# Optimization experiments

Measured on AMD Instinct MI355X. Metric: run time of the kernel, lower is better.

## Reference

```python
import jax, jax.numpy as jnp
import numpy as np

N = 500000       # total nodes
D = 256          # input_dim
H = 128          # hidden_dim
G = 4096         # number of graphs (batch.max()+1)


def setup_inputs() -> dict:
    key = jax.random.key(0)
    k_x, k_b, k_w1, k_b1, k_w2, k_b2 = jax.random.split(key, 6)
    x = jax.random.normal(k_x, (N, D), dtype=jnp.float32)
    batch = jnp.sort(jax.random.randint(k_b, (N,), 0, G)).astype(jnp.int64)
    batch = batch.at[-1].set(G - 1)  # ensure batch.max()+1 == G
    s1 = 1.0 / np.sqrt(D)
    s2 = 1.0 / np.sqrt(H)
    W1 = jax.random.uniform(k_w1, (D, H), jnp.float32, -s1, s1)
    b1 = jax.random.uniform(k_b1, (H,), jnp.float32, -s1, s1)
    W2 = jax.random.uniform(k_w2, (H, 1), jnp.float32, -s2, s2)
    b2 = jax.random.uniform(k_b2, (1,), jnp.float32, -s2, s2)
    return {"x": x, "batch": batch, "W1": W1, "b1": b1, "W2": W2, "b2": b2}


def reference(x, batch, W1, b1, W2, b2):
    # attention MLP: Linear -> Tanh -> Linear(->1)
    h = jnp.tanh(x @ W1 + b1)                  # [N, H]
    logits = (h @ W2 + b2)[:, 0]               # [N]
    # per-graph (segment) softmax over nodes
    m = jax.ops.segment_max(logits, batch, num_segments=G)       # [G]
    e = jnp.exp(logits - m[batch])                               # [N]
    denom = jax.ops.segment_sum(e, batch, num_segments=G)        # [G]
    w = e / denom[batch]                                         # [N]
    # weighted sum per graph; empty graphs -> zeros (matches torch branch)
    pooled = jax.ops.segment_sum(x * w[:, None], batch, num_segments=G)  # [G, D]
    return pooled
```

## Files before the change

### kernel.cpp

```cpp
#include <hip/hip_runtime.h>
#include <math.h>

#define D_DIM 256
#define H_DIM 128
#define TILE  32
#define HPAD  264

typedef __attribute__((ext_vector_type(8))) short bf16x8;
typedef __attribute__((ext_vector_type(4))) float f32x4;

__device__ __forceinline__ unsigned short f32_to_bf16(float f) {
  unsigned int u = __float_as_uint(f);
  u += 0x7FFFu + ((u >> 16) & 1u);
  return (unsigned short)(u >> 16);
}

__device__ __forceinline__ unsigned int pack_hi2(float f0, float f1, float& r0, float& r1) {
  unsigned int u0 = __float_as_uint(f0) & 0xFFFF0000u;
  unsigned int u1 = __float_as_uint(f1) & 0xFFFF0000u;
  r0 = f0 - __uint_as_float(u0);
  r1 = f1 - __uint_as_float(u1);
  return (u0 >> 16) | u1;
}
__device__ __forceinline__ unsigned int pack_lo2(float r0, float r1) {
  return (__float_as_uint(r0) >> 16) | (__float_as_uint(r1) & 0xFFFF0000u);
}

__device__ __forceinline__ float tanh_fast(float x) {
  float e = __expf(2.0f * x);
  return 1.0f - 2.0f / (e + 1.0f);
}

__global__ void setup_w1_kernel(const float* __restrict__ W1,
                                unsigned short* __restrict__ wfrag)
{
  const int t = threadIdx.x;
  const int l = t & 63, w = t >> 6;
  const int q = l >> 4, c = l & 15;
#pragma unroll
  for (int kt = 0; kt < 8; ++kt)
#pragma unroll
    for (int nt = 0; nt < 2; ++nt) {
      int f = kt * 2 + nt;
      int col = w * 32 + nt * 16 + c;
#pragma unroll
      for (int j = 0; j < 8; ++j) {
        int k = kt * 32 + q * 8 + j;
        wfrag[((size_t)f * 256 + t) * 8 + j] = f32_to_bf16(W1[k * H_DIM + col]);
      }
    }
}

__global__ void offsets_kernel(const void* __restrict__ batch, int* __restrict__ start,
                               int N, int G)
{
  int g = blockIdx.x * blockDim.x + threadIdx.x;
  if (g > G) return;
  const int* b32 = (const int*)batch;
  bool is64 = (b32[N - 1] != G - 1);
  int lo = 0, hi = N;
  while (lo < hi) {
    int mid = (lo + hi) >> 1;
    long long v = is64 ? ((const long long*)batch)[mid] : (long long)b32[mid];
    if (v < (long long)g) lo = mid + 1; else hi = mid;
  }
  start[g] = lo;
}

__global__ __launch_bounds__(256, 4)
void fused_kernel(const float* __restrict__ x, const unsigned short* __restrict__ wfrag,
                  const float* __restrict__ b1, const float* __restrict__ W2,
                  const int* __restrict__ start, float* __restrict__ out, int N)
{
  __shared__ unsigned short xhi[TILE][HPAD];
  __shared__ unsigned short xlo[TILE][HPAD];
  __shared__ float part[4][TILE];

  const int g = blockIdx.x;
  const int tid = threadIdx.x;
  const int s = start[g], e = start[g + 1];
  if (s >= e) { out[(size_t)g * D_DIM + tid] = 0.0f; return; }
  const int len = e - s;

  const int lane = tid & 63, w = tid >> 6;
  const int q = lane >> 4, c = lane & 15;

  bf16x8 wf[8][2];
#pragma unroll
  for (int kt = 0; kt < 8; ++kt)
#pragma unroll
    for (int nt = 0; nt < 2; ++nt)
      wf[kt][nt] = ((const bf16x8*)wfrag)[(kt * 2 + nt) * 256 + tid];

  float b1c[2], w2c[2];
#pragma unroll
  for (int nt = 0; nt < 2; ++nt) {
    int col = w * 32 + nt * 16 + c;
    b1c[nt] = b1[col];
    w2c[nt] = W2[col];
  }

  float m_run = -INFINITY, Z = 0.0f, accd = 0.0f;

  const int nT = (len + TILE - 1) / TILE;
  for (int ti = 0; ti < nT; ++ti) {
    const int t0 = ti * TILE;
    const int iend = min(TILE, len - t0);

#pragma unroll
    for (int it = 0; it < 4; ++it) {
      int id = tid + 256 * it;
      int row = id >> 5, col8 = (id & 31) * 8;
      int gr = min(s + t0 + row, N - 1);
      const float4* gp = reinterpret_cast<const float4*>(x + (size_t)gr * D_DIM + col8);
      float4 A = gp[0], B = gp[1];
      float r0, r1, r2, r3, r4, r5, r6, r7;
      uint4 H, L;
      H.x = pack_hi2(A.x, A.y, r0, r1);
      H.y = pack_hi2(A.z, A.w, r2, r3);
      H.z = pack_hi2(B.x, B.y, r4, r5);
      H.w = pack_hi2(B.z, B.w, r6, r7);
      L.x = pack_lo2(r0, r1);
      L.y = pack_lo2(r2, r3);
      L.z = pack_lo2(r4, r5);
      L.w = pack_lo2(r6, r7);
      *reinterpret_cast<uint4*>(&xhi[row][col8]) = H;
      *reinterpret_cast<uint4*>(&xlo[row][col8]) = L;
    }
    __syncthreads();

    f32x4 acc[2][2];
#pragma unroll
    for (int m = 0; m < 2; ++m)
#pragma unroll
      for (int nt = 0; nt < 2; ++nt) acc[m][nt] = (f32x4){0.f, 0.f, 0.f, 0.f};

#pragma unroll
    for (int kt = 0; kt < 8; ++kt) {
      const int koff = kt * 32 + q * 8;
      bf16x8 ah0 = *reinterpret_cast<const bf16x8*>(&xhi[c][koff]);
      bf16x8 al0 = *reinterpret_cast<const bf16x8*>(&xlo[c][koff]);
      bf16x8 ah1 = *reinterpret_cast<const bf16x8*>(&xhi[16 + c][koff]);
      bf16x8 al1 = *reinterpret_cast<const bf16x8*>(&xlo[16 + c][koff]);
#pragma unroll
      for (int nt = 0; nt < 2; ++nt) {
        acc[0][nt] = __builtin_amdgcn_mfma_f32_16x16x32_bf16(ah0, wf[kt][nt], acc[0][nt], 0, 0, 0);
        acc[0][nt] = __builtin_amdgcn_mfma_f32_16x16x32_bf16(al0, wf[kt][nt], acc[0][nt], 0, 0, 0);
        acc[1][nt] = __builtin_amdgcn_mfma_f32_16x16x32_bf16(ah1, wf[kt][nt], acc[1][nt], 0, 0, 0);
        acc[1][nt] = __builtin_amdgcn_mfma_f32_16x16x32_bf16(al1, wf[kt][nt], acc[1][nt], 0, 0, 0);
      }
    }

#pragma unroll
    for (int m = 0; m < 2; ++m)
#pragma unroll
      for (int r = 0; r < 4; ++r) {
        float v = tanh_fast(acc[m][0][r] + b1c[0]) * w2c[0]
                + tanh_fast(acc[m][1][r] + b1c[1]) * w2c[1];
#pragma unroll
        for (int o = 1; o < 16; o <<= 1) v += __shfl_xor(v, o, 64);
        if (c == 0) part[w][m * 16 + q * 4 + r] = v;
      }
    __syncthreads();

    {
      int i = lane & 31;
      float li = (i < iend) ? (part[0][i] + part[1][i] + part[2][i] + part[3][i])
                            : -INFINITY;
      float tmax = li;
#pragma unroll
      for (int o = 1; o < 64; o <<= 1) tmax = fmaxf(tmax, __shfl_xor(tmax, o, 64));
      float m_new = fmaxf(m_run, tmax);
      float ei = __expf(li - m_new);
      float esum = ei;
#pragma unroll
      for (int o = 1; o < 32; o <<= 1) esum += __shfl_xor(esum, o, 64);
      float scale = __expf(m_run - m_new);
      Z = Z * scale + esum;
      accd *= scale;
      for (int ii = 0; ii < iend; ++ii) {
        float ev = __shfl(ei, ii, 64);
        float xv = __uint_as_float((unsigned int)xhi[ii][tid] << 16)
                 + __uint_as_float((unsigned int)xlo[ii][tid] << 16);
        accd = fmaf(ev, xv, accd);
      }
      m_run = m_new;
    }
    __syncthreads();
  }

  out[(size_t)g * D_DIM + tid] = accd / Z;
}

extern "C" void kernel_launch(void* const* d_in, const int* in_sizes, int n_in,
                              void* d_out, int out_size, void* d_ws, size_t ws_size,
                              hipStream_t stream)
{
  const float* x     = (const float*)d_in[0];
  const void*  batch = d_in[1];
  const float* W1    = (const float*)d_in[2];
  const float* b1    = (const float*)d_in[3];
  const float* W2    = (const float*)d_in[4];

  const int N = in_sizes[0] / D_DIM;
  const int G = out_size / D_DIM;

  unsigned short* wfrag = (unsigned short*)d_ws;
  int* startA = (int*)((char*)d_ws + 16 * 256 * 8 * sizeof(unsigned short));
  float* out = (float*)d_out;

  setup_w1_kernel<<<1, 256, 0, stream>>>(W1, wfrag);
  offsets_kernel<<<(G + 1 + 255) / 256, 256, 0, stream>>>(batch, startA, N, G);
  fused_kernel<<<G, 256, 0, stream>>>(x, wfrag, b1, W2, startA, out, N);
}
```

Before: 200.6 us.

## Prefetch next node tile into registers while computing current tile

Result: slower. 450.0 us (+124.4%).

```diff
diff --git a/kernel.cpp b/kernel.cpp
--- a/kernel.cpp
+++ b/kernel.cpp
@@ -67,7 +67,7 @@
   start[g] = lo;
 }
 
-__global__ __launch_bounds__(256, 4)
+__global__ __launch_bounds__(256, 3)
 void fused_kernel(const float* __restrict__ x, const unsigned short* __restrict__ wfrag,
                   const float* __restrict__ b1, const float* __restrict__ W2,
                   const int* __restrict__ start, float* __restrict__ out, int N)
@@ -84,6 +84,7 @@
 
   const int lane = tid & 63, w = tid >> 6;
   const int q = lane >> 4, c = lane & 15;
+  const int srow = tid >> 5, scol8 = (tid & 31) * 8;
 
   bf16x8 wf[8][2];
 #pragma unroll
@@ -101,33 +102,42 @@
   }
 
   float m_run = -INFINITY, Z = 0.0f, accd = 0.0f;
-
   const int nT = (len + TILE - 1) / TILE;
+
+#pragma unroll
+  for (int it = 0; it < 4; ++it) {
+    int row = srow + it * 8;
+    int gr = min(s + row, N - 1);
+    const float4* gp = reinterpret_cast<const float4*>(x + (size_t)gr * D_DIM + scol8);
+    float4 A = gp[0], B = gp[1];
+    float r0, r1, r2, r3, r4, r5, r6, r7;
+    uint4 H, L;
+    H.x = pack_hi2(A.x, A.y, r0, r1);  H.y = pack_hi2(A.z, A.w, r2, r3);
+    H.z = pack_hi2(B.x, B.y, r4, r5);  H.w = pack_hi2(B.z, B.w, r6, r7);
+    L.x = pack_lo2(r0, r1);  L.y = pack_lo2(r2, r3);
+    L.z = pack_lo2(r4, r5);  L.w = pack_lo2(r6, r7);
+    *reinterpret_cast<uint4*>(&xhi[row][scol8]) = H;
+    *reinterpret_cast<uint4*>(&xlo[row][scol8]) = L;
+  }
+
   for (int ti = 0; ti < nT; ++ti) {
     const int t0 = ti * TILE;
     const int iend = min(TILE, len - t0);
-
-#pragma unroll
-    for (int it = 0; it < 4; ++it) {
-      int id = tid + 256 * it;
-      int row = id >> 5, col8 = (id & 31) * 8;
-      int gr = min(s + t0 + row, N - 1);
-      const float4* gp = reinterpret_cast<const float4*>(x + (size_t)gr * D_DIM + col8);
-      float4 A = gp[0], B = gp[1];
-      float r0, r1, r2, r3, r4, r5, r6, r7;
-      uint4 H, L;
-      H.x = pack_hi2(A.x, A.y, r0, r1);
-      H.y = pack_hi2(A.z, A.w, r2, r3);
-      H.z = pack_hi2(B.x, B.y, r4, r5);
-      H.w = pack_hi2(B.z, B.w, r6, r7);
-      L.x = pack_lo2(r0, r1);
-      L.y = pack_lo2(r2, r3);
-      L.z = pack_lo2(r4, r5);
-      L.w = pack_lo2(r6, r7);
-      *reinterpret_cast<uint4*>(&xhi[row][col8]) = H;
-      *reinterpret_cast<uint4*>(&xlo[row][col8]) = L;
-    }
+    const bool haveNext = (ti + 1 < nT);
+
     __syncthreads();
+
+    float4 pf[4][2];
+    if (haveNext) {
+#pragma unroll
+      for (int it = 0; it < 4; ++it) {
+        int row = srow + it * 8;
+        int gr = min(s + t0 + TILE + row, N - 1);
+        const float4* gp = reinterpret_cast<const float4*>(x + (size_t)gr * D_DIM + scol8);
+        pf[it][0] = gp[0];
+        pf[it][1] = gp[1];
+      }
+    }
 
     f32x4 acc[2][2];
 #pragma unroll
@@ -164,12 +174,12 @@
     __syncthreads();
 
     {
-      int i = lane & 31;
+      const int i = lane & 31;
       float li = (i < iend) ? (part[0][i] + part[1][i] + part[2][i] + part[3][i])
                             : -INFINITY;
       float tmax = li;
 #pragma unroll
-      for (int o = 1; o < 64; o <<= 1) tmax = fmaxf(tmax, __shfl_xor(tmax, o, 64));
+      for (int o = 1; o < 32; o <<= 1) tmax = fmaxf(tmax, __shfl_xor(tmax, o, 64));
       float m_new = fmaxf(m_run, tmax);
       float ei = __expf(li - m_new);
       float esum = ei;
@@ -177,16 +187,47 @@
       for (int o = 1; o < 32; o <<= 1) esum += __shfl_xor(esum, o, 64);
       float scale = __expf(m_run - m_new);
       Z = Z * scale + esum;
-      accd *= scale;
-      for (int ii = 0; ii < iend; ++ii) {
-        float ev = __shfl(ei, ii, 64);
-        float xv = __uint_as_float((unsigned int)xhi[ii][tid] << 16)
-                 + __uint_as_float((unsigned int)xlo[ii][tid] << 16);
-        accd = fmaf(ev, xv, accd);
-      }
+
+      float ac0 = 0.f, ac1 = 0.f, ac2 = 0.f, ac3 = 0.f;
+#pragma unroll
+      for (int ii = 0; ii < TILE; ii += 4) {
+        float e0 = __shfl(ei, ii + 0, 64);
+        float e1 = __shfl(ei, ii + 1, 64);
+        float e2 = __shfl(ei, ii + 2, 64);
+        float e3 = __shfl(ei, ii + 3, 64);
+        float x0 = __uint_as_float((unsigned int)xhi[ii + 0][tid] << 16)
+                 + __uint_as_float((unsigned int)xlo[ii + 0][tid] << 16);
+        float x1 = __uint_as_float((unsigned int)xhi[ii + 1][tid] << 16)
+                 + __uint_as_float((unsigned int)xlo[ii + 1][tid] << 16);
+        float x2 = __uint_as_float((unsigned int)xhi[ii + 2][tid] << 16)
+                 + __uint_as_float((unsigned int)xlo[ii + 2][tid] << 16);
+        float x3 = __uint_as_float((unsigned int)xhi[ii + 3][tid] << 16)
+                 + __uint_as_float((unsigned int)xlo[ii + 3][tid] << 16);
+        ac0 = fmaf(e0, x0, ac0);
+        ac1 = fmaf(e1, x1, ac1);
+        ac2 = fmaf(e2, x2, ac2);
+        ac3 = fmaf(e3, x3, ac3);
+      }
+      accd = fmaf(accd, scale, (ac0 + ac1) + (ac2 + ac3));
       m_run = m_new;
     }
     __syncthreads();
+
+    if (haveNext) {
+#pragma unroll
+      for (int it = 0; it < 4; ++it) {
+        int row = srow + it * 8;
+        float4 A = pf[it][0], B = pf[it][1];
+        float r0, r1, r2, r3, r4, r5, r6, r7;
+        uint4 H, L;
+        H.x = pack_hi2(A.x, A.y, r0, r1);  H.y = pack_hi2(A.z, A.w, r2, r3);
+        H.z = pack_hi2(B.x, B.y, r4, r5);  H.w = pack_hi2(B.z, B.w, r6, r7);
+        L.x = pack_lo2(r0, r1);  L.y = pack_lo2(r2, r3);
+        L.z = pack_lo2(r4, r5);  L.w = pack_lo2(r6, r7);
+        *reinterpret_cast<uint4*>(&xhi[row][scol8]) = H;
+        *reinterpret_cast<uint4*>(&xlo[row][scol8]) = L;
+      }
+    }
   }
 
   out[(size_t)g * D_DIM + tid] = accd / Z;
```

## Prefetch next x tile into registers, drop bf16 lo split, accumulate in fp32

Applied to the files above, without the earlier changes.

Measured after the change: 226.2 us. 12.8% more time.

```diff
diff --git a/kernel.cpp b/kernel.cpp
--- a/kernel.cpp
+++ b/kernel.cpp
@@ -15,15 +15,10 @@
   return (unsigned short)(u >> 16);
 }
 
-__device__ __forceinline__ unsigned int pack_hi2(float f0, float f1, float& r0, float& r1) {
-  unsigned int u0 = __float_as_uint(f0) & 0xFFFF0000u;
-  unsigned int u1 = __float_as_uint(f1) & 0xFFFF0000u;
-  r0 = f0 - __uint_as_float(u0);
-  r1 = f1 - __uint_as_float(u1);
+__device__ __forceinline__ unsigned int pack2_rn(float f0, float f1) {
+  unsigned int u0 = (__float_as_uint(f0) + 0x8000u) & 0xFFFF0000u;
+  unsigned int u1 = (__float_as_uint(f1) + 0x8000u) & 0xFFFF0000u;
   return (u0 >> 16) | u1;
-}
-__device__ __forceinline__ unsigned int pack_lo2(float r0, float r1) {
-  return (__float_as_uint(r0) >> 16) | (__float_as_uint(r1) & 0xFFFF0000u);
 }
 
 __device__ __forceinline__ float tanh_fast(float x) {
@@ -67,14 +62,14 @@
   start[g] = lo;
 }
 
-__global__ __launch_bounds__(256, 4)
+__global__ __launch_bounds__(256, 3)
 void fused_kernel(const float* __restrict__ x, const unsigned short* __restrict__ wfrag,
                   const float* __restrict__ b1, const float* __restrict__ W2,
                   const int* __restrict__ start, float* __restrict__ out, int N)
 {
   __shared__ unsigned short xhi[TILE][HPAD];
-  __shared__ unsigned short xlo[TILE][HPAD];
-  __shared__ float part[4][TILE];
+  __shared__ float part_t[TILE][4];
+  __shared__ float pacc_lds[8][D_DIM];
 
   const int g = blockIdx.x;
   const int tid = threadIdx.x;
@@ -84,92 +79,93 @@
 
   const int lane = tid & 63, w = tid >> 6;
   const int q = lane >> 4, c = lane & 15;
-
-  bf16x8 wf[8][2];
-#pragma unroll
-  for (int kt = 0; kt < 8; ++kt)
-#pragma unroll
-    for (int nt = 0; nt < 2; ++nt)
-      wf[kt][nt] = ((const bf16x8*)wfrag)[(kt * 2 + nt) * 256 + tid];
-
-  float b1c[2], w2c[2];
-#pragma unroll
-  for (int nt = 0; nt < 2; ++nt) {
-    int col = w * 32 + nt * 16 + c;
-    b1c[nt] = b1[col];
-    w2c[nt] = W2[col];
-  }
-
-  float m_run = -INFINITY, Z = 0.0f, accd = 0.0f;
+  const int srow = tid >> 5;
+  const int scol8 = (tid & 31) * 8;
+
+  const bf16x8* wfv = (const bf16x8*)wfrag;
+
+  float b1c0, b1c1, w2c0, w2c1;
+  {
+    int col0 = w * 32 + c, col1 = w * 32 + 16 + c;
+    b1c0 = b1[col0]; b1c1 = b1[col1];
+    w2c0 = W2[col0]; w2c1 = W2[col1];
+  }
+
+  float m_run = -INFINITY, Z = 0.0f;
+  float pc0 = 0.f, pc1 = 0.f, pc2 = 0.f, pc3 = 0.f,
+        pc4 = 0.f, pc5 = 0.f, pc6 = 0.f, pc7 = 0.f;
+
+  float4 A0, B0, A1, B1, A2, B2, A3, B3;
+  {
+    const float4* p0 = reinterpret_cast<const float4*>(x + (size_t)min(s + srow,      N - 1) * D_DIM + scol8);
+    const float4* p1 = reinterpret_cast<const float4*>(x + (size_t)min(s + srow +  8, N - 1) * D_DIM + scol8);
+    const float4* p2 = reinterpret_cast<const float4*>(x + (size_t)min(s + srow + 16, N - 1) * D_DIM + scol8);
+    const float4* p3 = reinterpret_cast<const float4*>(x + (size_t)min(s + srow + 24, N - 1) * D_DIM + scol8);
+    A0 = p0[0]; B0 = p0[1];
+    A1 = p1[0]; B1 = p1[1];
+    A2 = p2[0]; B2 = p2[1];
+    A3 = p3[0]; B3 = p3[1];
+  }
 
   const int nT = (len + TILE - 1) / TILE;
   for (int ti = 0; ti < nT; ++ti) {
-    const int t0 = ti * TILE;
-    const int iend = min(TILE, len - t0);
-
-#pragma unroll
-    for (int it = 0; it < 4; ++it) {
-      int id = tid + 256 * it;
-      int row = id >> 5, col8 = (id & 31) * 8;
-      int gr = min(s + t0 + row, N - 1);
-      const float4* gp = reinterpret_cast<const float4*>(x + (size_t)gr * D_DIM + col8);
-      float4 A = gp[0], B = gp[1];
-      float r0, r1, r2, r3, r4, r5, r6, r7;
-      uint4 H, L;
-      H.x = pack_hi2(A.x, A.y, r0, r1);
-      H.y = pack_hi2(A.z, A.w, r2, r3);
-      H.z = pack_hi2(B.x, B.y, r4, r5);
-      H.w = pack_hi2(B.z, B.w, r6, r7);
-      L.x = pack_lo2(r0, r1);
-      L.y = pack_lo2(r2, r3);
-      L.z = pack_lo2(r4, r5);
-      L.w = pack_lo2(r6, r7);
-      *reinterpret_cast<uint4*>(&xhi[row][col8]) = H;
-      *reinterpret_cast<uint4*>(&xlo[row][col8]) = L;
+    const int iend = min(TILE, len - ti * TILE);
+
+    {
+      uint4 H;
+      H.x = pack2_rn(A0.x, A0.y); H.y = pack2_rn(A0.z, A0.w);
+      H.z = pack2_rn(B0.x, B0.y); H.w = pack2_rn(B0.z, B0.w);
+      *reinterpret_cast<uint4*>(&xhi[srow][scol8]) = H;
+      H.x = pack2_rn(A1.x, A1.y); H.y = pack2_rn(A1.z, A1.w);
+      H.z = pack2_rn(B1.x, B1.y); H.w = pack2_rn(B1.z, B1.w);
+      *reinterpret_cast<uint4*>(&xhi[srow + 8][scol8]) = H;
+      H.x = pack2_rn(A2.x, A2.y); H.y = pack2_rn(A2.z, A2.w);
+      H.z = pack2_rn(B2.x, B2.y); H.w = pack2_rn(B2.z, B2.w);
+      *reinterpret_cast<uint4*>(&xhi[srow + 16][scol8]) = H;
+      H.x = pack2_rn(A3.x, A3.y); H.y = pack2_rn(A3.z, A3.w);
+      H.z = pack2_rn(B3.x, B3.y); H.w = pack2_rn(B3.z, B3.w);
+      *reinterpret_cast<uint4*>(&xhi[srow + 24][scol8]) = H;
     }
     __syncthreads();
 
-    f32x4 acc[2][2];
-#pragma unroll
-    for (int m = 0; m < 2; ++m)
-#pragma unroll
-      for (int nt = 0; nt < 2; ++nt) acc[m][nt] = (f32x4){0.f, 0.f, 0.f, 0.f};
-
+    f32x4 acc00 = {0.f, 0.f, 0.f, 0.f}, acc01 = {0.f, 0.f, 0.f, 0.f};
+    f32x4 acc10 = {0.f, 0.f, 0.f, 0.f}, acc11 = {0.f, 0.f, 0.f, 0.f};
 #pragma unroll
     for (int kt = 0; kt < 8; ++kt) {
       const int koff = kt * 32 + q * 8;
       bf16x8 ah0 = *reinterpret_cast<const bf16x8*>(&xhi[c][koff]);
-      bf16x8 al0 = *reinterpret_cast<const bf16x8*>(&xlo[c][koff]);
       bf16x8 ah1 = *reinterpret_cast<const bf16x8*>(&xhi[16 + c][koff]);
-      bf16x8 al1 = *reinterpret_cast<const bf16x8*>(&xlo[16 + c][koff]);
-#pragma unroll
-      for (int nt = 0; nt < 2; ++nt) {
-        acc[0][nt] = __builtin_amdgcn_mfma_f32_16x16x32_bf16(ah0, wf[kt][nt], acc[0][nt], 0, 0, 0);
-        acc[0][nt] = __builtin_amdgcn_mfma_f32_16x16x32_bf16(al0, wf[kt][nt], acc[0][nt], 0, 0, 0);
-        acc[1][nt] = __builtin_amdgcn_mfma_f32_16x16x32_bf16(ah1, wf[kt][nt], acc[1][nt], 0, 0, 0);
-        acc[1][nt] = __builtin_amdgcn_mfma_f32_16x16x32_bf16(al1, wf[kt][nt], acc[1][nt], 0, 0, 0);
-      }
-    }
-
-#pragma unroll
-    for (int m = 0; m < 2; ++m)
-#pragma unroll
-      for (int r = 0; r < 4; ++r) {
-        float v = tanh_fast(acc[m][0][r] + b1c[0]) * w2c[0]
-                + tanh_fast(acc[m][1][r] + b1c[1]) * w2c[1];
-#pragma unroll
-        for (int o = 1; o < 16; o <<= 1) v += __shfl_xor(v, o, 64);
-        if (c == 0) part[w][m * 16 + q * 4 + r] = v;
-      }
+      bf16x8 bf0 = wfv[(kt * 2 + 0) * 256 + tid];
+      bf16x8 bf1 = wfv[(kt * 2 + 1) * 256 + tid];
+      acc00 = __builtin_amdgcn_mfma_f32_16x16x32_bf16(ah0, bf0, acc00, 0, 0, 0);
+      acc01 = __builtin_amdgcn_mfma_f32_16x16x32_bf16(ah0, bf1, acc01, 0, 0, 0);
+      acc10 = __builtin_amdgcn_mfma_f32_16x16x32_bf16(ah1, bf0, acc10, 0, 0, 0);
+      acc11 = __builtin_amdgcn_mfma_f32_16x16x32_bf16(ah1, bf1, acc11, 0, 0, 0);
+    }
+
+#pragma unroll
+    for (int r = 0; r < 4; ++r) {
+      float v = tanh_fast(acc00[r] + b1c0) * w2c0 + tanh_fast(acc01[r] + b1c1) * w2c1;
+#pragma unroll
+      for (int o = 1; o < 16; o <<= 1) v += __shfl_xor(v, o, 64);
+      if (c == 0) part_t[q * 4 + r][w] = v;
+    }
+#pragma unroll
+    for (int r = 0; r < 4; ++r) {
+      float v = tanh_fast(acc10[r] + b1c0) * w2c0 + tanh_fast(acc11[r] + b1c1) * w2c1;
+#pragma unroll
+      for (int o = 1; o < 16; o <<= 1) v += __shfl_xor(v, o, 64);
+      if (c == 0) part_t[16 + q * 4 + r][w] = v;
+    }
     __syncthreads();
 
     {
-      int i = lane & 31;
-      float li = (i < iend) ? (part[0][i] + part[1][i] + part[2][i] + part[3][i])
-                            : -INFINITY;
+      const int i = lane & 31;
+      float4 pp = *reinterpret_cast<const float4*>(&part_t[i][0]);
+      float li = (i < iend) ? (pp.x + pp.y + pp.z + pp.w) : -INFINITY;
       float tmax = li;
 #pragma unroll
-      for (int o = 1; o < 64; o <<= 1) tmax = fmaxf(tmax, __shfl_xor(tmax, o, 64));
+      for (int o = 1; o < 32; o <<= 1) tmax = fmaxf(tmax, __shfl_xor(tmax, o, 64));
       float m_new = fmaxf(m_run, tmax);
       float ei = __expf(li - m_new);
       float esum = ei;
@@ -177,19 +173,52 @@
       for (int o = 1; o < 32; o <<= 1) esum += __shfl_xor(esum, o, 64);
       float scale = __expf(m_run - m_new);
       Z = Z * scale + esum;
-      accd *= scale;
-      for (int ii = 0; ii < iend; ++ii) {
-        float ev = __shfl(ei, ii, 64);
-        float xv = __uint_as_float((unsigned int)xhi[ii][tid] << 16)
-                 + __uint_as_float((unsigned int)xlo[ii][tid] << 16);
-        accd = fmaf(ev, xv, accd);
-      }
       m_run = m_new;
-    }
-    __syncthreads();
-  }
-
-  out[(size_t)g * D_DIM + tid] = accd / Z;
+
+      float e0 = __shfl(ei, srow,      64);
+      float e1 = __shfl(ei, srow +  8, 64);
+      float e2 = __shfl(ei, srow + 16, 64);
+      float e3 = __shfl(ei, srow + 24, 64);
+      pc0 *= scale; pc1 *= scale; pc2 *= scale; pc3 *= scale;
+      pc4 *= scale; pc5 *= scale; pc6 *= scale; pc7 *= scale;
+      pc0 = fmaf(e0, A0.x, pc0); pc1 = fmaf(e0, A0.y, pc1);
+      pc2 = fmaf(e0, A0.z, pc2); pc3 = fmaf(e0, A0.w, pc3);
+      pc4 = fmaf(e0, B0.x, pc4); pc5 = fmaf(e0, B0.y, pc5);
+      pc6 = fmaf(e0, B0.z, pc6); pc7 = fmaf(e0, B0.w, pc7);
+      pc0 = fmaf(e1, A1.x, pc0); pc1 = fmaf(e1, A1.y, pc1);
+      pc2 = fmaf(e1, A1.z, pc2); pc3 = fmaf(e1, A1.w, pc3);
+      pc4 = fmaf(e1, B1.x, pc4); pc5 = fmaf(e1, B1.y, pc5);
+      pc6 = fmaf(e1, B1.z, pc6); pc7 = fmaf(e1, B1.w, pc7);
+      pc0 = fmaf(e2, A2.x, pc0); pc1 = fmaf(e2, A2.y, pc1);
+      pc2 = fmaf(e2, A2.z, pc2); pc3 = fmaf(e2, A2.w, pc3);
+      pc4 = fmaf(e2, B2.x, pc4); pc5 = fmaf(e2, B2.y, pc5);
+      pc6 = fmaf(e2, B2.z, pc6); pc7 = fmaf(e2, B2.w, pc7);
+      pc0 = fmaf(e3, A3.x, pc0); pc1 = fmaf(e3, A3.y, pc1);
+      pc2 = fmaf(e3, A3.z, pc2); pc3 = fmaf(e3, A3.w, pc3);
+      pc4 = fmaf(e3, B3.x, pc4); pc5 = fmaf(e3, B3.y, pc5);
+      pc6 = fmaf(e3, B3.z, pc6); pc7 = fmaf(e3, B3.w, pc7);
+    }
+
+    {
+      const int nb = s + (ti + 1) * TILE;
+      const float4* p0 = reinterpret_cast<const float4*>(x + (size_t)min(nb + srow,      N - 1) * D_DIM + scol8);
+      const float4* p1 = reinterpret_cast<const float4*>(x + (size_t)min(nb + srow +  8, N - 1) * D_DIM + scol8);
+      const float4* p2 = reinterpret_cast<const float4*>(x + (size_t)min(nb + srow + 16, N - 1) * D_DIM + scol8);
+      const float4* p3 = reinterpret_cast<const float4*>(x + (size_t)min(nb + srow + 24, N - 1) * D_DIM + scol8);
+      A0 = p0[0]; B0 = p0[1];
+      A1 = p1[0]; B1 = p1[1];
+      A2 = p2[0]; B2 = p2[1];
+      A3 = p3[0]; B3 = p3[1];
+    }
+  }
+
+  *reinterpret_cast<float4*>(&pacc_lds[srow][scol8])     = make_float4(pc0, pc1, pc2, pc3);
+  *reinterpret_cast<float4*>(&pacc_lds[srow][scol8 + 4]) = make_float4(pc4, pc5, pc6, pc7);
+  __syncthreads();
+  float sum = 0.f;
+#pragma unroll
+  for (int r = 0; r < 8; ++r) sum += pacc_lds[r][tid];
+  out[(size_t)g * D_DIM + tid] = sum / Z;
 }
 
 extern "C" void kernel_launch(void* const* d_in, const int* in_sizes, int n_in,
```
